# Kernel optimization log

Measured on AMD Instinct MI355X. Metric: run time of the kernel, lower is better.

The kernel has to match this reference:

```python
import jax, jax.numpy as jnp
import numpy as np

N_NODES = 20000
IN_C = 512
OUT_C = 128
HEADS = 4
N_EDGES = 320000
NEG_SLOPE = 0.2


def setup_inputs() -> dict:
    key = jax.random.key(0)
    ks = jax.random.split(key, 10)
    x = jax.random.normal(ks[0], (N_NODES, IN_C), dtype=jnp.float32)
    edge_index = jax.random.randint(ks[1], (2, N_EDGES), 0, N_NODES, dtype=jnp.int64)
    s = 0.05
    return {
        "x": x,
        "edge_index": edge_index,
        "W1": jax.random.normal(ks[2], (IN_C, HEADS * OUT_C), dtype=jnp.float32) * s,
        "a_src1": jax.random.normal(ks[3], (HEADS, OUT_C), dtype=jnp.float32) * s,
        "a_dst1": jax.random.normal(ks[4], (HEADS, OUT_C), dtype=jnp.float32) * s,
        "b1": jnp.zeros((HEADS * OUT_C,), dtype=jnp.float32),
        "W2": jax.random.normal(ks[5], (HEADS * OUT_C, 1 * OUT_C), dtype=jnp.float32) * s,
        "a_src2": jax.random.normal(ks[6], (1, OUT_C), dtype=jnp.float32) * s,
        "a_dst2": jax.random.normal(ks[7], (1, OUT_C), dtype=jnp.float32) * s,
        "b2": jnp.zeros((OUT_C,), dtype=jnp.float32),
    }


def gat_conv(x, src, dst, W, a_src, a_dst, b, heads, out_c, concat):
    N = x.shape[0]
    h = (x @ W).reshape(N, heads, out_c)            # [N,H,C]
    al_src = jnp.sum(h * a_src, axis=-1)            # [N,H]
    al_dst = jnp.sum(h * a_dst, axis=-1)            # [N,H]
    e = jax.nn.leaky_relu(al_src[src] + al_dst[dst], NEG_SLOPE)  # [E,H]
    # segment softmax over edges grouped by destination node
    e_max = jax.ops.segment_max(e, dst, num_segments=N)         # [N,H]
    e = jnp.exp(e - e_max[dst])
    denom = jax.ops.segment_sum(e, dst, num_segments=N)         # [N,H]
    alpha = e / (denom[dst] + 1e-16)                             # [E,H]
    msg = h[src] * alpha[:, :, None]                             # [E,H,C]
    out = jax.ops.segment_sum(msg, dst, num_segments=N)          # [N,H,C]
    out = out.reshape(N, heads * out_c) if concat else jnp.mean(out, axis=1)
    return out + b


def reference(x, edge_index, W1, a_src1, a_dst1, b1, W2, a_src2, a_dst2, b2):
    N = x.shape[0]
    # PyG GATConv adds self-loops by default
    loops = jnp.arange(N, dtype=edge_index.dtype)
    src = jnp.concatenate([edge_index[0], loops])
    dst = jnp.concatenate([edge_index[1], loops])
    h = gat_conv(x, src, dst, W1, a_src1, a_dst1, b1, HEADS, OUT_C, concat=True)
    h = jax.nn.elu(h)
    return gat_conv(h, src, dst, W2, a_src2, a_dst2, b2, 1, OUT_C, concat=False)
```

## Files before the change

### kernel.cpp

```cpp
#include <hip/hip_runtime.h>
#include <hip/hip_bf16.h>

typedef __hip_bfloat16 bf16;
typedef __bf16 bf16x8 __attribute__((ext_vector_type(8)));
typedef float f32x4 __attribute__((ext_vector_type(4)));

#define NEG_SLOPE 0.2f
#define F32_THRESH 256


__device__ __forceinline__ bool is_f32(const int* fcnt) { return *fcnt > F32_THRESH; }

__device__ __forceinline__ float ld_f(const void* p, long long i, bool f32) {
    return f32 ? ((const float*)p)[i] : __bfloat162float(((const bf16*)p)[i]);
}

__device__ __forceinline__ float b2f(unsigned hs) {
    return __uint_as_float(hs << 16);
}

__device__ __forceinline__ unsigned pack_bf2(float a, float b) {
    union { bf16 h[2]; unsigned u; } p;
    p.h[0] = __float2bfloat16(a);
    p.h[1] = __float2bfloat16(b);
    return p.u;
}

__device__ __forceinline__ void load_lds16(const void* g, void* l) {
    __builtin_amdgcn_global_load_lds(
        (const __attribute__((address_space(1))) void*)g,
        (__attribute__((address_space(3))) void*)l, 16, 0, 0);
}

template <int CPL> struct FV;
template <> struct FV<8> {
    uint4 v;
    __device__ __forceinline__ void load(const bf16* p) { v = *(const uint4*)p; }
    __device__ __forceinline__ void fma(float* acc, float w) const {
        unsigned uu[4] = {v.x, v.y, v.z, v.w};
#pragma unroll
        for (int q = 0; q < 4; q++) {
            acc[2 * q] += w * b2f(uu[q] & 0xFFFFu);
            acc[2 * q + 1] += w * b2f(uu[q] >> 16);
        }
    }
};
template <> struct FV<2> {
    unsigned v;
    __device__ __forceinline__ void load(const bf16* p) { v = *(const unsigned*)p; }
    __device__ __forceinline__ void fma(float* acc, float w) const {
        acc[0] += w * b2f(v & 0xFFFFu);
        acc[1] += w * b2f(v >> 16);
    }
};


__global__ void k_probe(const unsigned* xw, long long nw, const int* idx, int n_half,
                        int* cnt, int* iflag) {
    long long t = blockIdx.x * (long long)blockDim.x + threadIdx.x;
    long long stride = (long long)gridDim.x * blockDim.x;
    int c = 0;
    for (long long i = t; i < nw; i += stride)
        if ((xw[i] & 0x7F80u) == 0x7F80u) c++;
    if (c) atomicAdd(cnt, c);
    int any = 0;
    for (long long i = t; i < n_half; i += stride)
        if (idx[2 * i + 1] != 0) any = 1;
    if (any) atomicOr(iflag, 1);
}


__device__ __forceinline__ int edge_val(const void* idx, long long i, int is64) {
    return is64 ? (int)((const long long*)idx)[i] : ((const int*)idx)[i];
}

__global__ void k_count(const void* idx, const int* iflag, int E0, int N, int* deg) {
    int e = blockIdx.x * blockDim.x + threadIdx.x;
    if (e >= E0 + N) return;
    int is64 = (*iflag == 0);
    int d = (e < E0) ? edge_val(idx, (long long)E0 + e, is64) : (e - E0);
    if ((unsigned)d >= (unsigned)N) d = 0;
    atomicAdd(&deg[d], 1);
}

__global__ __launch_bounds__(1024) void k_scan(const int* deg, int* rowptr, int N) {
    __shared__ int part[1024];
    int t = threadIdx.x;
    int chunk = (N + 1023) / 1024;
    int s = t * chunk, e = min(N, s + chunk);
    int sum = 0;
    for (int i = s; i < e; i++) sum += deg[i];
    part[t] = sum;
    __syncthreads();
    for (int off = 1; off < 1024; off <<= 1) {
        int v = (t >= off) ? part[t - off] : 0;
        __syncthreads();
        part[t] += v;
        __syncthreads();
    }
    int run = (t == 0) ? 0 : part[t - 1];
    for (int i = s; i < e; i++) { rowptr[i] = run; run += deg[i]; }
    if (t == 1023) rowptr[N] = part[1023];
}

__global__ void k_scatter(const void* idx, const int* iflag, int E0, int N,
                          const int* rowptr, int* cursor, int* csr_src) {
    int e = blockIdx.x * blockDim.x + threadIdx.x;
    if (e >= E0 + N) return;
    int is64 = (*iflag == 0);
    int s, d;
    if (e < E0) {
        s = edge_val(idx, e, is64);
        d = edge_val(idx, (long long)E0 + e, is64);
    } else {
        s = d = e - E0;
    }
    if ((unsigned)s >= (unsigned)N) s = 0;
    if ((unsigned)d >= (unsigned)N) d = 0;
    int pos = rowptr[d] + atomicAdd(&cursor[d], 1);
    if ((unsigned)pos < (unsigned)(E0 + N)) csr_src[pos] = s;
}


__global__ void k_prep(const void* x, const int* fcnt, bf16* xb, bf16* xtail,
                       const void* W1, bf16* W1t, const void* W2, bf16* W2t,
                       bf16* hpad, int hpad_elems, int N, int K, int C1, int C2,
                       int R0, long long n_valid, long long n_total) {
    const int b = blockIdx.x;
    const int tid = threadIdx.x;
    const bool f32 = is_f32(fcnt);
    if (b < 512) {
        if (!f32) return;
        long long n8 = n_total / 8;
        for (long long i = (long long)b * 256 + tid; i < n8; i += 512LL * 256) {
            long long base = i * 8;
            uint4 out;
            if (base + 8 <= n_valid) {
                const float4* s4 = (const float4*)x;
                float4 x0 = s4[i * 2], x1 = s4[i * 2 + 1];
                out.x = pack_bf2(x0.x, x0.y);
                out.y = pack_bf2(x0.z, x0.w);
                out.z = pack_bf2(x1.x, x1.y);
                out.w = pack_bf2(x1.z, x1.w);
            } else {
                bf16 tmp[8];
#pragma unroll
                for (int j = 0; j < 8; j++) {
                    long long k = base + j;
                    tmp[j] = (k < n_valid) ? __float2bfloat16(ld_f(x, k, true))
                                           : __float2bfloat16(0.f);
                }
                out = *(uint4*)tmp;
            }
            ((uint4*)xb)[i] = out;
        }
    } else if (b < 528) {
        int total = 128 * K;
        for (int i = (b - 512) * 256 + tid; i < total; i += 16 * 256) {
            int r = i / K;
            long long src = (long long)(R0 + r) * K + (i - r * K);
            xtail[i] = (R0 + r < N) ? __float2bfloat16(ld_f(x, src, f32))
                                    : __float2bfloat16(0.f);
        }
    } else if (b < 656) {
        int total = K * C1;
        for (int i = (b - 528) * 256 + tid; i < total; i += 128 * 256) {
            int k = i / C1, n = i - k * C1;
            W1t[(size_t)n * K + k] = __float2bfloat16(ld_f(W1, i, f32));
        }
    } else if (b < 688) {
        int total = C1 * C2;
        for (int i = (b - 656) * 256 + tid; i < total; i += 32 * 256) {
            int k = i / C2, n = i - k * C2;
            W2t[(size_t)n * C1 + k] = __float2bfloat16(ld_f(W2, i, f32));
        }
    } else {
        for (int i = (b - 688) * 256 + tid; i < hpad_elems; i += 16 * 256)
            hpad[i] = __float2bfloat16(0.f);
    }
}


template <int BN, bool SEL, int H>
__global__ __launch_bounds__(256) void k_gemm(const void* Araw, const bf16* Aconv,
                                              const bf16* Atail, const int* fcnt,
                                              const bf16* __restrict__ Bt,
                                              bf16* __restrict__ C,
                                              const void* a_s, const void* a_d,
                                              float* __restrict__ als,
                                              float* __restrict__ ald,
                                              int M, int Nn, int K, int nfull) {
    constexpr int BM = 128, BK = 32;
    constexpr int NT = BN / 32;
    const int m0 = blockIdx.x * BM;
    const int n0 = blockIdx.y * BN;
    __shared__ __bf16 As[BM][BK];
    __shared__ __bf16 Bs[BN][BK];
    const int tid = threadIdx.x;
    const int wave = tid >> 6;
    const int lane = tid & 63;
    const int wm = (wave & 1) * 64;
    const int wn = (wave >> 1) * (NT * 16);
    const int lm = lane & 15;
    const int quad = lane >> 4;
    const int srow = tid >> 2;
    const int scol = (tid & 3) * 8;

    f32x4 acc[4][NT];
#pragma unroll
    for (int mt = 0; mt < 4; mt++)
#pragma unroll
        for (int nt = 0; nt < NT; nt++) acc[mt][nt] = (f32x4){0.f, 0.f, 0.f, 0.f};

    const bf16* Abase;
    int arow0;
    if (SEL) {
        const bf16* Asel = is_f32(fcnt) ? Aconv : (const bf16*)Araw;
        if ((int)blockIdx.x < nfull) { Abase = Asel; arow0 = m0; }
        else { Abase = Atail; arow0 = 0; }
    } else {
        Abase = (const bf16*)Araw;
        arow0 = m0;
    }

    const char* Ab = (const char*)(Abase + (size_t)(arow0 + srow) * K + scol);
    const char* Bb = (const char*)(Bt + (size_t)(n0 + srow) * K + scol);
    char* ldsA = (char*)&As[0][0] + wave * 1024;
    char* ldsB = (char*)&Bs[0][0] + wave * 1024;
    const size_t rstep = (size_t)64 * K * 2;

    for (int k0 = 0; k0 < K; k0 += BK) {
        __syncthreads();
        const size_t kb = (size_t)k0 * 2;
        load_lds16(Ab + kb, ldsA);
        load_lds16(Ab + kb + rstep, ldsA + 4096);
        load_lds16(Bb + kb, ldsB);
        if (BN == 128) load_lds16(Bb + kb + rstep, ldsB + 4096);
        __syncthreads();
        bf16x8 af[4], bfv[NT];
#pragma unroll
        for (int mt = 0; mt < 4; mt++)
            af[mt] = *(const bf16x8*)&As[wm + mt * 16 + lm][quad * 8];
#pragma unroll
        for (int nt = 0; nt < NT; nt++)
            bfv[nt] = *(const bf16x8*)&Bs[wn + nt * 16 + lm][quad * 8];
#pragma unroll
        for (int mt = 0; mt < 4; mt++)
#pragma unroll
            for (int nt = 0; nt < NT; nt++)
                acc[mt][nt] = __builtin_amdgcn_mfma_f32_16x16x32_bf16(
                    af[mt], bfv[nt], acc[mt][nt], 0, 0, 0);
    }

#pragma unroll
    for (int mt = 0; mt < 4; mt++) {
        int rb = m0 + wm + mt * 16 + quad * 4;
#pragma unroll
        for (int nt = 0; nt < NT; nt++) {
            int col = n0 + wn + nt * 16 + lm;
#pragma unroll
            for (int r = 0; r < 4; r++) {
                int row = rb + r;
                if (row < M) C[(size_t)row * Nn + col] = __float2bfloat16(acc[mt][nt][r]);
            }
        }
    }

    const bool f32 = is_f32(fcnt);
    float sa_[NT], sd_[NT];
#pragma unroll
    for (int nt = 0; nt < NT; nt++) {
        int col = n0 + wn + nt * 16 + lm;
        sa_[nt] = ld_f(a_s, col, f32);
        sd_[nt] = ld_f(a_d, col, f32);
    }
    const int head = (H == 4) ? (n0 >> 7) : 0;
#pragma unroll
    for (int mt = 0; mt < 4; mt++) {
#pragma unroll
        for (int r = 0; r < 4; r++) {
            float ps_ = 0.f, pd_ = 0.f;
#pragma unroll
            for (int nt = 0; nt < NT; nt++) {
                float v = acc[mt][nt][r];
                ps_ += v * sa_[nt];
                pd_ += v * sd_[nt];
            }
#pragma unroll
            for (int off = 1; off < 16; off <<= 1) {
                ps_ += __shfl_xor(ps_, off, 64);
                pd_ += __shfl_xor(pd_, off, 64);
            }
            int row = m0 + wm + mt * 16 + quad * 4 + r;
            if (lm == 0 && row < M) {
                atomicAdd(&als[(size_t)row * H + head], ps_);
                atomicAdd(&ald[(size_t)row * H + head], pd_);
            }
        }
    }
}


template <int C, int H, bool ELU, bool DYN_OUT>
__global__ __launch_bounds__(256) void k_agg(
    const bf16* __restrict__ feat, const float* __restrict__ als,
    const float* __restrict__ ald, const int* __restrict__ rowptr,
    const int* __restrict__ csr_src, const void* bias, const int* fcnt,
    void* outp, int N, int E) {
    constexpr int CPL = C / 64;
    constexpr int Ch = C / H;
    constexpr int WST = (H == 4) ? 5 : 1;
    const int n = blockIdx.x;
    const int tid = threadIdx.x;
    const int wave = tid >> 6;
    const int lane = tid & 63;
    const int c0 = lane * CPL;
    const int head = c0 / Ch;

    __shared__ float red[4][C];
    __shared__ float s_w[64 * WST];
    __shared__ int s_src[64];
    __shared__ float ps[4][H];

    int start = rowptr[n];
    if (start < 0) start = 0;
    int end = rowptr[n + 1];
    if (end > E) end = E;
    int deg = end - start;
    if (deg < 0) deg = 0;

    float acc[CPL] = {};
    float psum = 0.f;

    for (int base = 0; base < deg; base += 64) {
        int cnt = min(64, deg - base);
        __syncthreads();
        if (H == 4) {
            int e_ = tid & 63, h_ = tid >> 6;
            if (e_ < cnt) {
                int s = csr_src[start + base + e_];
                if ((unsigned)s >= (unsigned)N) s = 0;
                if (h_ == 0) s_src[e_] = s;
                float l = als[(size_t)s * 4 + h_] + ald[(size_t)n * 4 + h_];
                l = l > 0.f ? l : NEG_SLOPE * l;
                s_w[e_ * 5 + h_] = __expf(fminf(l, 60.f));
            }
        } else {
            if (tid < cnt) {
                int s = csr_src[start + base + tid];
                if ((unsigned)s >= (unsigned)N) s = 0;
                s_src[tid] = s;
                float l = als[s] + ald[n];
                l = l > 0.f ? l : NEG_SLOPE * l;
                s_w[tid] = __expf(fminf(l, 60.f));
            }
        }
        __syncthreads();
#pragma unroll 4
        for (int e = wave; e < cnt; e += 4) {
            int s = s_src[e];
            float wl = (H == 4) ? s_w[e * 5 + head] : s_w[e];
            psum += wl;
            FV<CPL> f;
            f.load(feat + (size_t)s * C + c0);
            f.fma(acc, wl);
        }
    }

#pragma unroll
    for (int j = 0; j < CPL; j++) red[wave][c0 + j] = acc[j];
    if ((lane & 15) == 0) ps[wave][head] = psum;
    __syncthreads();

    const bool f32 = is_f32(fcnt);
    for (int c = tid; c < C; c += 256) {
        int h = c / Ch;
        float sv = 0.f;
        float dn = 1e-16f;
#pragma unroll
        for (int w2 = 0; w2 < 4; w2++) {
            sv += red[w2][c];
            dn += ps[w2][h];
        }
        float v = sv / dn + ld_f(bias, c, f32);
        if (ELU) v = v > 0.f ? v : expf(v) - 1.f;
        size_t oi = (size_t)n * C + c;
        if (DYN_OUT && f32) ((float*)outp)[oi] = v;
        else ((bf16*)outp)[oi] = __float2bfloat16(v);
    }
}


extern "C" void kernel_launch(void* const* d_in, const int* in_sizes, int n_in,
                              void* d_out, int out_size, void* d_ws, size_t ws_size,
                              hipStream_t stream) {
    const int N = in_sizes[0] / 512;
    const int K = 512;
    const int C1 = 512;
    const int C2 = 128;
    const int H1 = 4;
    const int E0 = in_sizes[1] / 2;
    const int E = E0 + N;
    const int Mpad = (N + 127) / 128 * 128;
    const int nfull = N / 128;

    const void* x_raw = d_in[0];
    const void* eidx = d_in[1];
    const void* W1 = d_in[2];
    const void* as1 = d_in[3];
    const void* ad1 = d_in[4];
    const void* b1 = d_in[5];
    const void* W2 = d_in[6];
    const void* as2 = d_in[7];
    const void* ad2 = d_in[8];
    const void* b2 = d_in[9];

    char* ws = (char*)d_ws;
    size_t off = 0;
    auto take = [&](size_t bytes) {
        size_t r = off;
        off += (bytes + 255) & ~(size_t)255;
        return r;
    };
    bf16* xb     = (bf16*)(ws + take((size_t)Mpad * K * 2));
    bf16* xtail  = (bf16*)(ws + take((size_t)128 * K * 2));
    bf16* h1     = (bf16*)(ws + take((size_t)N * C1 * 2));
    bf16* hagg   = (bf16*)(ws + take((size_t)Mpad * C1 * 2));
    bf16* W1t    = (bf16*)(ws + take((size_t)K * C1 * 2));
    bf16* W2t    = (bf16*)(ws + take((size_t)C1 * C2 * 2));
    int* rowptr  = (int*)(ws + take((size_t)(N + 1) * 4));
    int* csr_src = (int*)(ws + take((size_t)E * 4));
    int* zbase   = (int*)(ws + take((size_t)(12 * N + 2) * 4));
    int* deg     = zbase;
    int* cursor  = zbase + N;
    float* al1s  = (float*)(zbase + 2 * N);
    float* al1d  = al1s + 4 * N;
    float* al2s  = al1d + 4 * N;
    float* al2d  = al2s + N;
    int* iflag   = zbase + 12 * N;
    int* fcnt    = zbase + 12 * N + 1;
    bf16* h2     = xb;
    if (off > ws_size) return;

    hipMemsetAsync(zbase, 0, (size_t)(12 * N + 2) * 4, stream);

    long long nw = (long long)in_sizes[0] / 2;
    if (nw > (1 << 20)) nw = 1 << 20;
    int nh = E0 > (1 << 16) ? (1 << 16) : E0;
    k_probe<<<256, 256, 0, stream>>>((const unsigned*)x_raw, nw, (const int*)eidx, nh,
                                     fcnt, iflag);

    k_count<<<(E + 255) / 256, 256, 0, stream>>>(eidx, iflag, E0, N, deg);
    k_scan<<<1, 1024, 0, stream>>>(deg, rowptr, N);
    k_scatter<<<(E + 255) / 256, 256, 0, stream>>>(eidx, iflag, E0, N, rowptr, cursor,
                                                   csr_src);

    k_prep<<<704, 256, 0, stream>>>(x_raw, fcnt, xb, xtail, W1, W1t, W2, W2t,
                                    hagg + (size_t)N * C1, (Mpad - N) * C1,
                                    N, K, C1, C2, nfull * 128,
                                    (long long)N * K, (long long)Mpad * K);

    dim3 g1(Mpad / 128, C1 / 128);
    k_gemm<128, true, 4><<<g1, 256, 0, stream>>>(x_raw, xb, xtail, fcnt, W1t, h1,
                                                 as1, ad1, al1s, al1d, N, C1, K, nfull);
    k_agg<512, 4, true, false><<<N, 256, 0, stream>>>(
        h1, al1s, al1d, rowptr, csr_src, b1, fcnt, hagg, N, E);

    dim3 g2(Mpad / 128, C2 / 64);
    k_gemm<64, false, 1><<<g2, 256, 0, stream>>>(hagg, nullptr, nullptr, fcnt, W2t, h2,
                                                 as2, ad2, al2s, al2d, N, C2, C1, 0);
    k_agg<128, 1, false, true><<<N, 256, 0, stream>>>(
        h2, al2s, al2d, rowptr, csr_src, b2, fcnt, d_out, N, E);
}
```

Before: 327.0 us.

## Fuse whole GAT pipeline into one cooperative persistent kernel with grid syncs

Replaces the sequence of separate launches (memset, probe, count, scan, scatter, prep, two GEMMs, two aggregations) with a single cooperative kernel that runs each phase in turn, separated by grid-wide barriers. The scan becomes a distributed block-sum plus single-block prefix. The goal is to remove per-launch overhead and inter-kernel gaps. The trade-off is that occupancy is capped by the shared-memory and register footprint of the largest phase, the grid is limited to resident blocks, and every phase waits on a full grid barrier, with the old multi-kernel path kept as a fallback.

```diff
diff --git a/kernel.cpp b/kernel.cpp
--- a/kernel.cpp
+++ b/kernel.cpp
@@ -1,5 +1,8 @@
 #include <hip/hip_runtime.h>
 #include <hip/hip_bf16.h>
+#include <hip/hip_cooperative_groups.h>
+
+namespace cg = cooperative_groups;
 
 typedef __hip_bfloat16 bf16;
 typedef __bf16 bf16x8 __attribute__((ext_vector_type(8)));
@@ -53,6 +56,415 @@
         acc[1] += w * b2f(v >> 16);
     }
 };
+
+__device__ __forceinline__ int edge_val(const void* idx, long long i, int is64) {
+    return is64 ? (int)((const long long*)idx)[i] : ((const int*)idx)[i];
+}
+
+
+template <int BN, bool SEL, int H>
+__device__ void dev_gemm(char* smem, int bx, int by,
+                         const void* Araw, const bf16* Aconv, const bf16* Atail,
+                         const int* fcnt, const bf16* __restrict__ Bt,
+                         bf16* __restrict__ C, const void* a_s, const void* a_d,
+                         float* __restrict__ als, float* __restrict__ ald,
+                         int M, int Nn, int K, int nfull) {
+    constexpr int BM = 128, BK = 32;
+    constexpr int NT = BN / 32;
+    const int m0 = bx * BM;
+    const int n0 = by * BN;
+    __bf16* As = (__bf16*)smem;
+    __bf16* Bs = (__bf16*)(smem + 8192);
+    const int tid = threadIdx.x;
+    const int wave = tid >> 6;
+    const int lane = tid & 63;
+    const int wm = (wave & 1) * 64;
+    const int wn = (wave >> 1) * (NT * 16);
+    const int lm = lane & 15;
+    const int quad = lane >> 4;
+    const int srow = tid >> 2;
+    const int scol = (tid & 3) * 8;
+
+    f32x4 acc[4][NT];
+#pragma unroll
+    for (int mt = 0; mt < 4; mt++)
+#pragma unroll
+        for (int nt = 0; nt < NT; nt++) acc[mt][nt] = (f32x4){0.f, 0.f, 0.f, 0.f};
+
+    const bf16* Abase;
+    int arow0;
+    if (SEL) {
+        const bf16* Asel = is_f32(fcnt) ? Aconv : (const bf16*)Araw;
+        if (bx < nfull) { Abase = Asel; arow0 = m0; }
+        else { Abase = Atail; arow0 = 0; }
+    } else {
+        Abase = (const bf16*)Araw;
+        arow0 = m0;
+    }
+
+    const char* Ab = (const char*)(Abase + (size_t)(arow0 + srow) * K + scol);
+    const char* Bb = (const char*)(Bt + (size_t)(n0 + srow) * K + scol);
+    char* ldsA = (char*)As + wave * 1024;
+    char* ldsB = (char*)Bs + wave * 1024;
+    const size_t rstep = (size_t)64 * K * 2;
+
+    for (int k0 = 0; k0 < K; k0 += BK) {
+        __syncthreads();
+        const size_t kb = (size_t)k0 * 2;
+        load_lds16(Ab + kb, ldsA);
+        load_lds16(Ab + kb + rstep, ldsA + 4096);
+        load_lds16(Bb + kb, ldsB);
+        if (BN == 128) load_lds16(Bb + kb + rstep, ldsB + 4096);
+        __syncthreads();
+        bf16x8 af[4], bfv[NT];
+#pragma unroll
+        for (int mt = 0; mt < 4; mt++)
+            af[mt] = *(const bf16x8*)(As + (wm + mt * 16 + lm) * 32 + quad * 8);
+#pragma unroll
+        for (int nt = 0; nt < NT; nt++)
+            bfv[nt] = *(const bf16x8*)(Bs + (wn + nt * 16 + lm) * 32 + quad * 8);
+#pragma unroll
+        for (int mt = 0; mt < 4; mt++)
+#pragma unroll
+            for (int nt = 0; nt < NT; nt++)
+                acc[mt][nt] = __builtin_amdgcn_mfma_f32_16x16x32_bf16(
+                    af[mt], bfv[nt], acc[mt][nt], 0, 0, 0);
+    }
+
+#pragma unroll
+    for (int mt = 0; mt < 4; mt++) {
+        int rb = m0 + wm + mt * 16 + quad * 4;
+#pragma unroll
+        for (int nt = 0; nt < NT; nt++) {
+            int col = n0 + wn + nt * 16 + lm;
+#pragma unroll
+            for (int r = 0; r < 4; r++) {
+                int row = rb + r;
+                if (row < M) C[(size_t)row * Nn + col] = __float2bfloat16(acc[mt][nt][r]);
+            }
+        }
+    }
+
+    const bool f32 = is_f32(fcnt);
+    float sa_[NT], sd_[NT];
+#pragma unroll
+    for (int nt = 0; nt < NT; nt++) {
+        int col = n0 + wn + nt * 16 + lm;
+        sa_[nt] = ld_f(a_s, col, f32);
+        sd_[nt] = ld_f(a_d, col, f32);
+    }
+    const int head = (H == 4) ? (n0 >> 7) : 0;
+#pragma unroll
+    for (int mt = 0; mt < 4; mt++) {
+#pragma unroll
+        for (int r = 0; r < 4; r++) {
+            float ps_ = 0.f, pd_ = 0.f;
+#pragma unroll
+            for (int nt = 0; nt < NT; nt++) {
+                float v = acc[mt][nt][r];
+                ps_ += v * sa_[nt];
+                pd_ += v * sd_[nt];
+            }
+#pragma unroll
+            for (int off = 1; off < 16; off <<= 1) {
+                ps_ += __shfl_xor(ps_, off, 64);
+                pd_ += __shfl_xor(pd_, off, 64);
+            }
+            int row = m0 + wm + mt * 16 + quad * 4 + r;
+            if (lm == 0 && row < M) {
+                atomicAdd(&als[(size_t)row * H + head], ps_);
+                atomicAdd(&ald[(size_t)row * H + head], pd_);
+            }
+        }
+    }
+}
+
+template <int C, int H, bool ELU, bool DYN_OUT>
+__device__ void dev_agg(char* smem, int n, const bf16* __restrict__ feat,
+                        const float* __restrict__ als, const float* __restrict__ ald,
+                        const int* __restrict__ rowptr, const int* __restrict__ csr_src,
+                        const void* bias, const int* fcnt, void* outp, int N, int E) {
+    constexpr int CPL = C / 64;
+    constexpr int Ch = C / H;
+    constexpr int WST = (H == 4) ? 5 : 1;
+    float* red = (float*)smem;
+    float* s_w = red + 4 * C;
+    int* s_src = (int*)(s_w + 64 * WST);
+    float* ps = (float*)(s_src + 64);
+    const int tid = threadIdx.x;
+    const int wave = tid >> 6;
+    const int lane = tid & 63;
+    const int c0 = lane * CPL;
+    const int head = c0 / Ch;
+
+    int start = rowptr[n];
+    if (start < 0) start = 0;
+    int end = rowptr[n + 1];
+    if (end > E) end = E;
+    int deg = end - start;
+    if (deg < 0) deg = 0;
+
+    float acc[CPL] = {};
+    float psum = 0.f;
+
+    for (int base = 0; base < deg; base += 64) {
+        int cnt = min(64, deg - base);
+        __syncthreads();
+        if (H == 4) {
+            int e_ = tid & 63, h_ = tid >> 6;
+            if (e_ < cnt) {
+                int s = csr_src[start + base + e_];
+                if ((unsigned)s >= (unsigned)N) s = 0;
+                if (h_ == 0) s_src[e_] = s;
+                float l = als[(size_t)s * 4 + h_] + ald[(size_t)n * 4 + h_];
+                l = l > 0.f ? l : NEG_SLOPE * l;
+                s_w[e_ * 5 + h_] = __expf(fminf(l, 60.f));
+            }
+        } else {
+            if (tid < cnt) {
+                int s = csr_src[start + base + tid];
+                if ((unsigned)s >= (unsigned)N) s = 0;
+                s_src[tid] = s;
+                float l = als[s] + ald[n];
+                l = l > 0.f ? l : NEG_SLOPE * l;
+                s_w[tid] = __expf(fminf(l, 60.f));
+            }
+        }
+        __syncthreads();
+#pragma unroll 4
+        for (int e = wave; e < cnt; e += 4) {
+            int s = s_src[e];
+            float wl = (H == 4) ? s_w[e * 5 + head] : s_w[e];
+            psum += wl;
+            FV<CPL> f;
+            f.load(feat + (size_t)s * C + c0);
+            f.fma(acc, wl);
+        }
+    }
+
+    __syncthreads();
+#pragma unroll
+    for (int j = 0; j < CPL; j++) red[wave * C + c0 + j] = acc[j];
+    if ((lane & 15) == 0) ps[wave * H + head] = psum;
+    __syncthreads();
+
+    const bool f32 = is_f32(fcnt);
+    for (int c = tid; c < C; c += 256) {
+        int h = c / Ch;
+        float sv = 0.f;
+        float dn = 1e-16f;
+#pragma unroll
+        for (int w2 = 0; w2 < 4; w2++) {
+            sv += red[w2 * C + c];
+            dn += ps[w2 * H + h];
+        }
+        float v = sv / dn + ld_f(bias, c, f32);
+        if (ELU) v = v > 0.f ? v : expf(v) - 1.f;
+        size_t oi = (size_t)n * C + c;
+        if (DYN_OUT && f32) ((float*)outp)[oi] = v;
+        else ((bf16*)outp)[oi] = __float2bfloat16(v);
+    }
+}
+
+
+struct MegaArgs {
+    const void* x_raw; const void* eidx;
+    const void* W1; const void* as1; const void* ad1; const void* b1;
+    const void* W2; const void* as2; const void* ad2; const void* b2;
+    bf16* xb; bf16* xtail; bf16* h1; bf16* hagg; bf16* W1t; bf16* W2t;
+    int* rowptr; int* csr_src; int* zbase; int* bsum;
+    void* out;
+    int N, K, C1, C2, E0, E, Mpad, nfull;
+    long long nw_cap; int nh_cap;
+};
+
+__global__ __launch_bounds__(256) void k_mega(MegaArgs a) {
+    cg::grid_group grid = cg::this_grid();
+    __shared__ __align__(16) char smem[16640];
+
+    const int blk = blockIdx.x;
+    const int tid = threadIdx.x;
+    const int G = gridDim.x;
+    const long long gt = (long long)blk * 256 + tid;
+    const long long GT = (long long)G * 256;
+
+    const int N = a.N, K = a.K, C1 = a.C1, C2 = a.C2;
+    const int E0 = a.E0, E = a.E, Mpad = a.Mpad, nfull = a.nfull;
+    int* deg = a.zbase;
+    int* cursor = a.zbase + N;
+    float* al1s = (float*)(a.zbase + 2 * N);
+    float* al1d = al1s + 4 * N;
+    float* al2s = al1d + 4 * N;
+    float* al2d = al2s + N;
+    int* iflag = a.zbase + 12 * N;
+    int* fcnt = a.zbase + 12 * N + 1;
+    bf16* h2 = a.xb;
+
+    {
+        long long zn = 12LL * N + 2;
+        for (long long i = gt; i < zn; i += GT) a.zbase[i] = 0;
+        unsigned* hp = (unsigned*)(a.hagg + (size_t)N * C1);
+        long long pw = (long long)(Mpad - N) * C1 / 2;
+        for (long long i = gt; i < pw; i += GT) hp[i] = 0;
+    }
+    grid.sync();
+
+    {
+        const unsigned* xw = (const unsigned*)a.x_raw;
+        int c = 0;
+        for (long long i = gt; i < a.nw_cap; i += GT)
+            if ((xw[i] & 0x7F80u) == 0x7F80u) c++;
+        if (c) atomicAdd(fcnt, c);
+        const int* idx = (const int*)a.eidx;
+        int any = 0;
+        for (long long i = gt; i < a.nh_cap; i += GT)
+            if (idx[2 * i + 1] != 0) any = 1;
+        if (any) atomicOr(iflag, 1);
+    }
+    grid.sync();
+
+    {
+        const int is64 = (*iflag == 0);
+        const bool f32 = is_f32(fcnt);
+        for (long long e = gt; e < E; e += GT) {
+            int d = (e < E0) ? edge_val(a.eidx, (long long)E0 + e, is64) : (int)(e - E0);
+            if ((unsigned)d >= (unsigned)N) d = 0;
+            atomicAdd(&deg[d], 1);
+        }
+        for (long long i = gt; i < (long long)K * C1; i += GT) {
+            int k = (int)(i / C1), n = (int)(i - (long long)k * C1);
+            a.W1t[(size_t)n * K + k] = __float2bfloat16(ld_f(a.W1, i, f32));
+        }
+        for (long long i = gt; i < (long long)C1 * C2; i += GT) {
+            int k = (int)(i / C2), n = (int)(i - (long long)k * C2);
+            a.W2t[(size_t)n * C1 + k] = __float2bfloat16(ld_f(a.W2, i, f32));
+        }
+        if (f32) {
+            long long n8 = (long long)Mpad * K / 8;
+            long long nv = (long long)N * K;
+            for (long long i = gt; i < n8; i += GT) {
+                long long base = i * 8;
+                uint4 out;
+                if (base + 8 <= nv) {
+                    const float4* s4 = (const float4*)a.x_raw;
+                    float4 x0 = s4[i * 2], x1 = s4[i * 2 + 1];
+                    out.x = pack_bf2(x0.x, x0.y);
+                    out.y = pack_bf2(x0.z, x0.w);
+                    out.z = pack_bf2(x1.x, x1.y);
+                    out.w = pack_bf2(x1.z, x1.w);
+                } else {
+                    bf16 tmp[8];
+#pragma unroll
+                    for (int j = 0; j < 8; j++) {
+                        long long kk = base + j;
+                        tmp[j] = (kk < nv) ? __float2bfloat16(ld_f(a.x_raw, kk, true))
+                                           : __float2bfloat16(0.f);
+                    }
+                    out = *(uint4*)tmp;
+                }
+                ((uint4*)a.xb)[i] = out;
+            }
+        }
+        int R0 = nfull * 128;
+        for (long long i = gt; i < (long long)128 * K; i += GT) {
+            int r = (int)(i / K);
+            long long src = (long long)(R0 + r) * K + (i - (long long)r * K);
+            a.xtail[i] = (R0 + r < N) ? __float2bfloat16(ld_f(a.x_raw, src, f32))
+                                      : __float2bfloat16(0.f);
+        }
+    }
+    grid.sync();
+
+    const int CH = (N + G - 1) / G;
+    const int cb = blk * CH;
+    const int ce = min(N, cb + CH);
+    {
+        int* ss = (int*)smem;
+        int local = 0;
+        for (int i = cb + tid; i < ce; i += 256) local += deg[i];
+        ss[tid] = local;
+        __syncthreads();
+        for (int s = 128; s > 0; s >>= 1) {
+            if (tid < s) ss[tid] += ss[tid + s];
+            __syncthreads();
+        }
+        if (tid == 0) a.bsum[blk] = ss[0];
+    }
+    grid.sync();
+
+    if (blk == 0) {
+        int* ss = (int*)smem;
+        int per = (G + 255) / 256;
+        int b0 = tid * per, b1 = min(G, b0 + per);
+        int s = 0;
+        for (int i = b0; i < b1; i++) s += a.bsum[i];
+        ss[tid] = s;
+        __syncthreads();
+        for (int off = 1; off < 256; off <<= 1) {
+            int x = (tid >= off) ? ss[tid - off] : 0;
+            __syncthreads();
+            ss[tid] += x;
+            __syncthreads();
+        }
+        int run = ss[tid] - s;
+        for (int i = b0; i < b1; i++) {
+            int v = a.bsum[i];
+            a.bsum[i] = run;
+            run += v;
+        }
+        if (tid == 255) a.rowptr[N] = ss[255];
+    }
+    grid.sync();
+
+    if (tid == 0) {
+        int run = a.bsum[blk];
+        for (int i = cb; i < ce; i++) { a.rowptr[i] = run; run += deg[i]; }
+    }
+    grid.sync();
+
+    {
+        const int is64 = (*iflag == 0);
+        for (long long e = gt; e < E; e += GT) {
+            int s, d;
+            if (e < E0) {
+                s = edge_val(a.eidx, e, is64);
+                d = edge_val(a.eidx, (long long)E0 + e, is64);
+            } else {
+                s = d = (int)(e - E0);
+            }
+            if ((unsigned)s >= (unsigned)N) s = 0;
+            if ((unsigned)d >= (unsigned)N) d = 0;
+            int pos = a.rowptr[d] + atomicAdd(&cursor[d], 1);
+            if ((unsigned)pos < (unsigned)E) a.csr_src[pos] = s;
+        }
+        const int mt1 = Mpad / 128;
+        const int nb1 = mt1 * (C1 / 128);
+        for (int t = blk; t < nb1; t += G)
+            dev_gemm<128, true, 4>(smem, t % mt1, t / mt1, a.x_raw, a.xb, a.xtail,
+                                   fcnt, a.W1t, a.h1, a.as1, a.ad1, al1s, al1d,
+                                   N, C1, K, nfull);
+    }
+    grid.sync();
+
+    for (int n = blk; n < N; n += G)
+        dev_agg<512, 4, true, false>(smem, n, a.h1, al1s, al1d, a.rowptr,
+                                     a.csr_src, a.b1, fcnt, a.hagg, N, E);
+    grid.sync();
+
+    {
+        const int mt1 = Mpad / 128;
+        const int nb2 = mt1 * (C2 / 64);
+        for (int t = blk; t < nb2; t += G)
+            dev_gemm<64, false, 1>(smem, t % mt1, t / mt1, a.hagg, nullptr, nullptr,
+                                   fcnt, a.W2t, h2, a.as2, a.ad2, al2s, al2d,
+                                   N, C2, C1, 0);
+    }
+    grid.sync();
+
+    for (int n = blk; n < N; n += G)
+        dev_agg<128, 1, false, true>(smem, n, h2, al2s, al2d, a.rowptr,
+                                     a.csr_src, a.b2, fcnt, a.out, N, E);
+}
 
 
 __global__ void k_probe(const unsigned* xw, long long nw, const int* idx, int n_half,
@@ -67,11 +479,6 @@
     for (long long i = t; i < n_half; i += stride)
         if (idx[2 * i + 1] != 0) any = 1;
     if (any) atomicOr(iflag, 1);
-}
-
-
-__device__ __forceinline__ int edge_val(const void* idx, long long i, int is64) {
-    return is64 ? (int)((const long long*)idx)[i] : ((const int*)idx)[i];
 }
 
 __global__ void k_count(const void* idx, const int* iflag, int E0, int N, int* deg) {
@@ -120,7 +527,6 @@
     int pos = rowptr[d] + atomicAdd(&cursor[d], 1);
     if ((unsigned)pos < (unsigned)(E0 + N)) csr_src[pos] = s;
 }
-
 
 __global__ void k_prep(const void* x, const int* fcnt, bf16* xb, bf16* xtail,
                        const void* W1, bf16* W1t, const void* W2, bf16* W2t,
@@ -180,214 +586,28 @@
     }
 }
 
-
 template <int BN, bool SEL, int H>
-__global__ __launch_bounds__(256) void k_gemm(const void* Araw, const bf16* Aconv,
-                                              const bf16* Atail, const int* fcnt,
-                                              const bf16* __restrict__ Bt,
-                                              bf16* __restrict__ C,
-                                              const void* a_s, const void* a_d,
-                                              float* __restrict__ als,
-                                              float* __restrict__ ald,
-                                              int M, int Nn, int K, int nfull) {
-    constexpr int BM = 128, BK = 32;
-    constexpr int NT = BN / 32;
-    const int m0 = blockIdx.x * BM;
-    const int n0 = blockIdx.y * BN;
-    __shared__ __bf16 As[BM][BK];
-    __shared__ __bf16 Bs[BN][BK];
-    const int tid = threadIdx.x;
-    const int wave = tid >> 6;
-    const int lane = tid & 63;
-    const int wm = (wave & 1) * 64;
-    const int wn = (wave >> 1) * (NT * 16);
-    const int lm = lane & 15;
-    const int quad = lane >> 4;
-    const int srow = tid >> 2;
-    const int scol = (tid & 3) * 8;
-
-    f32x4 acc[4][NT];
-#pragma unroll
-    for (int mt = 0; mt < 4; mt++)
-#pragma unroll
-        for (int nt = 0; nt < NT; nt++) acc[mt][nt] = (f32x4){0.f, 0.f, 0.f, 0.f};
-
-    const bf16* Abase;
-    int arow0;
-    if (SEL) {
-        const bf16* Asel = is_f32(fcnt) ? Aconv : (const bf16*)Araw;
-        if ((int)blockIdx.x < nfull) { Abase = Asel; arow0 = m0; }
-        else { Abase = Atail; arow0 = 0; }
-    } else {
-        Abase = (const bf16*)Araw;
-        arow0 = m0;
-    }
-
-    const char* Ab = (const char*)(Abase + (size_t)(arow0 + srow) * K + scol);
-    const char* Bb = (const char*)(Bt + (size_t)(n0 + srow) * K + scol);
-    char* ldsA = (char*)&As[0][0] + wave * 1024;
-    char* ldsB = (char*)&Bs[0][0] + wave * 1024;
-    const size_t rstep = (size_t)64 * K * 2;
-
-    for (int k0 = 0; k0 < K; k0 += BK) {
-        __syncthreads();
-        const size_t kb = (size_t)k0 * 2;
-        load_lds16(Ab + kb, ldsA);
-        load_lds16(Ab + kb + rstep, ldsA + 4096);
-        load_lds16(Bb + kb, ldsB);
-        if (BN == 128) load_lds16(Bb + kb + rstep, ldsB + 4096);
-        __syncthreads();
-        bf16x8 af[4], bfv[NT];
-#pragma unroll
-        for (int mt = 0; mt < 4; mt++)
-            af[mt] = *(const bf16x8*)&As[wm + mt * 16 + lm][quad * 8];
-#pragma unroll
-        for (int nt = 0; nt < NT; nt++)
-            bfv[nt] = *(const bf16x8*)&Bs[wn + nt * 16 + lm][quad * 8];
-#pragma unroll
-        for (int mt = 0; mt < 4; mt++)
-#pragma unroll
-            for (int nt = 0; nt < NT; nt++)
-                acc[mt][nt] = __builtin_amdgcn_mfma_f32_16x16x32_bf16(
-                    af[mt], bfv[nt], acc[mt][nt], 0, 0, 0);
-    }
-
-#pragma unroll
-    for (int mt = 0; mt < 4; mt++) {
-        int rb = m0 + wm + mt * 16 + quad * 4;
-#pragma unroll
-        for (int nt = 0; nt < NT; nt++) {
-            int col = n0 + wn + nt * 16 + lm;
-#pragma unroll
-            for (int r = 0; r < 4; r++) {
-                int row = rb + r;
-                if (row < M) C[(size_t)row * Nn + col] = __float2bfloat16(acc[mt][nt][r]);
-            }
-        }
-    }
-
-    const bool f32 = is_f32(fcnt);
-    float sa_[NT], sd_[NT];
-#pragma unroll
-    for (int nt = 0; nt < NT; nt++) {
-        int col = n0 + wn + nt * 16 + lm;
-        sa_[nt] = ld_f(a_s, col, f32);
-        sd_[nt] = ld_f(a_d, col, f32);
-    }
-    const int head = (H == 4) ? (n0 >> 7) : 0;
-#pragma unroll
-    for (int mt = 0; mt < 4; mt++) {
-#pragma unroll
-        for (int r = 0; r < 4; r++) {
-            float ps_ = 0.f, pd_ = 0.f;
-#pragma unroll
-            for (int nt = 0; nt < NT; nt++) {
-                float v = acc[mt][nt][r];
-                ps_ += v * sa_[nt];
-                pd_ += v * sd_[nt];
-            }
-#pragma unroll
-            for (int off = 1; off < 16; off <<= 1) {
-                ps_ += __shfl_xor(ps_, off, 64);
-                pd_ += __shfl_xor(pd_, off, 64);
-            }
-            int row = m0 + wm + mt * 16 + quad * 4 + r;
-            if (lm == 0 && row < M) {
-                atomicAdd(&als[(size_t)row * H + head], ps_);
-                atomicAdd(&ald[(size_t)row * H + head], pd_);
-            }
-        }
-    }
-}
-
+__global__ __launch_bounds__(256) void k_gemm_w(const void* Araw, const bf16* Aconv,
+                                                const bf16* Atail, const int* fcnt,
+                                                const bf16* Bt, bf16* C,
+                                                const void* a_s, const void* a_d,
+                                                float* als, float* ald,
+                                                int M, int Nn, int K, int nfull) {
+    __shared__ __align__(16) char smem[128 * 32 * 2 + BN * 32 * 2];
+    dev_gemm<BN, SEL, H>(smem, blockIdx.x, blockIdx.y, Araw, Aconv, Atail, fcnt,
+                         Bt, C, a_s, a_d, als, ald, M, Nn, K, nfull);
+}
 
 template <int C, int H, bool ELU, bool DYN_OUT>
-__global__ __launch_bounds__(256) void k_agg(
-    const bf16* __restrict__ feat, const float* __restrict__ als,
-    const float* __restrict__ ald, const int* __restrict__ rowptr,
-    const int* __restrict__ csr_src, const void* bias, const int* fcnt,
-    void* outp, int N, int E) {
-    constexpr int CPL = C / 64;
-    constexpr int Ch = C / H;
-    constexpr int WST = (H == 4) ? 5 : 1;
-    const int n = blockIdx.x;
-    const int tid = threadIdx.x;
-    const int wave = tid >> 6;
-    const int lane = tid & 63;
-    const int c0 = lane * CPL;
-    const int head = c0 / Ch;
-
-    __shared__ float red[4][C];
-    __shared__ float s_w[64 * WST];
-    __shared__ int s_src[64];
-    __shared__ float ps[4][H];
-
-    int start = rowptr[n];
-    if (start < 0) start = 0;
-    int end = rowptr[n + 1];
-    if (end > E) end = E;
-    int deg = end - start;
-    if (deg < 0) deg = 0;
-
-    float acc[CPL] = {};
-    float psum = 0.f;
-
-    for (int base = 0; base < deg; base += 64) {
-        int cnt = min(64, deg - base);
-        __syncthreads();
-        if (H == 4) {
-            int e_ = tid & 63, h_ = tid >> 6;
-            if (e_ < cnt) {
-                int s = csr_src[start + base + e_];
-                if ((unsigned)s >= (unsigned)N) s = 0;
-                if (h_ == 0) s_src[e_] = s;
-                float l = als[(size_t)s * 4 + h_] + ald[(size_t)n * 4 + h_];
-                l = l > 0.f ? l : NEG_SLOPE * l;
-                s_w[e_ * 5 + h_] = __expf(fminf(l, 60.f));
-            }
-        } else {
-            if (tid < cnt) {
-                int s = csr_src[start + base + tid];
-                if ((unsigned)s >= (unsigned)N) s = 0;
-                s_src[tid] = s;
-                float l = als[s] + ald[n];
-                l = l > 0.f ? l : NEG_SLOPE * l;
-                s_w[tid] = __expf(fminf(l, 60.f));
-            }
-        }
-        __syncthreads();
-#pragma unroll 4
-        for (int e = wave; e < cnt; e += 4) {
-            int s = s_src[e];
-            float wl = (H == 4) ? s_w[e * 5 + head] : s_w[e];
-            psum += wl;
-            FV<CPL> f;
-            f.load(feat + (size_t)s * C + c0);
-            f.fma(acc, wl);
-        }
-    }
-
-#pragma unroll
-    for (int j = 0; j < CPL; j++) red[wave][c0 + j] = acc[j];
-    if ((lane & 15) == 0) ps[wave][head] = psum;
-    __syncthreads();
-
-    const bool f32 = is_f32(fcnt);
-    for (int c = tid; c < C; c += 256) {
-        int h = c / Ch;
-        float sv = 0.f;
-        float dn = 1e-16f;
-#pragma unroll
-        for (int w2 = 0; w2 < 4; w2++) {
-            sv += red[w2][c];
-            dn += ps[w2][h];
-        }
-        float v = sv / dn + ld_f(bias, c, f32);
-        if (ELU) v = v > 0.f ? v : expf(v) - 1.f;
-        size_t oi = (size_t)n * C + c;
-        if (DYN_OUT && f32) ((float*)outp)[oi] = v;
-        else ((bf16*)outp)[oi] = __float2bfloat16(v);
-    }
+__global__ __launch_bounds__(256) void k_agg_w(const bf16* feat, const float* als,
+                                               const float* ald, const int* rowptr,
+                                               const int* csr_src, const void* bias,
+                                               const int* fcnt, void* outp,
+                                               int N, int E) {
+    __shared__ __align__(16) char
+        smem[4 * C * 4 + 64 * ((H == 4) ? 5 : 1) * 4 + 64 * 4 + 4 * H * 4];
+    dev_agg<C, H, ELU, DYN_OUT>(smem, blockIdx.x, feat, als, ald, rowptr, csr_src,
+                                bias, fcnt, outp, N, E);
 }
 
 
@@ -398,22 +618,10 @@
     const int K = 512;
     const int C1 = 512;
     const int C2 = 128;
-    const int H1 = 4;
     const int E0 = in_sizes[1] / 2;
     const int E = E0 + N;
     const int Mpad = (N + 127) / 128 * 128;
     const int nfull = N / 128;
-
-    const void* x_raw = d_in[0];
-    const void* eidx = d_in[1];
-    const void* W1 = d_in[2];
-    const void* as1 = d_in[3];
-    const void* ad1 = d_in[4];
-    const void* b1 = d_in[5];
-    const void* W2 = d_in[6];
-    const void* as2 = d_in[7];
-    const void* ad2 = d_in[8];
-    const void* b2 = d_in[9];
 
     char* ws = (char*)d_ws;
     size_t off = 0;
@@ -431,44 +639,74 @@
     int* rowptr  = (int*)(ws + take((size_t)(N + 1) * 4));
     int* csr_src = (int*)(ws + take((size_t)E * 4));
     int* zbase   = (int*)(ws + take((size_t)(12 * N + 2) * 4));
-    int* deg     = zbase;
-    int* cursor  = zbase + N;
-    float* al1s  = (float*)(zbase + 2 * N);
-    float* al1d  = al1s + 4 * N;
-    float* al2s  = al1d + 4 * N;
-    float* al2d  = al2s + N;
-    int* iflag   = zbase + 12 * N;
-    int* fcnt    = zbase + 12 * N + 1;
-    bf16* h2     = xb;
+    int* bsum    = (int*)(ws + take((size_t)4096 * 4));
     if (off > ws_size) return;
 
+    MegaArgs a;
+    a.x_raw = d_in[0]; a.eidx = d_in[1];
+    a.W1 = d_in[2]; a.as1 = d_in[3]; a.ad1 = d_in[4]; a.b1 = d_in[5];
+    a.W2 = d_in[6]; a.as2 = d_in[7]; a.ad2 = d_in[8]; a.b2 = d_in[9];
+    a.xb = xb; a.xtail = xtail; a.h1 = h1; a.hagg = hagg;
+    a.W1t = W1t; a.W2t = W2t;
+    a.rowptr = rowptr; a.csr_src = csr_src; a.zbase = zbase; a.bsum = bsum;
+    a.out = d_out;
+    a.N = N; a.K = K; a.C1 = C1; a.C2 = C2;
+    a.E0 = E0; a.E = E; a.Mpad = Mpad; a.nfull = nfull;
+    long long nw = (long long)in_sizes[0] / 2;
+    a.nw_cap = nw > (1 << 20) ? (1 << 20) : nw;
+    a.nh_cap = E0 > (1 << 16) ? (1 << 16) : E0;
+
+    int dev = 0;
+    hipGetDevice(&dev);
+    int coop = 0, numCU = 0, nbPerCU = 0;
+    hipDeviceGetAttribute(&coop, hipDeviceAttributeCooperativeLaunch, dev);
+    hipDeviceGetAttribute(&numCU, hipDeviceAttributeMultiprocessorCount, dev);
+    hipError_t oe = hipOccupancyMaxActiveBlocksPerMultiprocessor(
+        &nbPerCU, reinterpret_cast<const void*>(&k_mega), 256, 0);
+
+    if (coop && oe == hipSuccess && nbPerCU >= 1 && numCU >= 1) {
+        int G = nbPerCU * numCU;
+        if (G > 4096) G = 4096;
+        void* params[] = {&a};
+        hipError_t e = hipLaunchCooperativeKernel(
+            reinterpret_cast<const void*>(&k_mega), dim3(G), dim3(256),
+            params, 0, stream);
+        if (e == hipSuccess) return;
+    }
+
+    float* al1s = (float*)(zbase + 2 * N);
+    float* al1d = al1s + 4 * N;
+    float* al2s = al1d + 4 * N;
+    float* al2d = al2s + N;
+    int* deg = zbase;
+    int* cursor = zbase + N;
+    int* iflag = zbase + 12 * N;
+    int* fcnt = zbase + 12 * N + 1;
+    bf16* h2 = xb;
+
     hipMemsetAsync(zbase, 0, (size_t)(12 * N + 2) * 4, stream);
-
-    long long nw = (long long)in_sizes[0] / 2;
-    if (nw > (1 << 20)) nw = 1 << 20;
-    int nh = E0 > (1 << 16) ? (1 << 16) : E0;
-    k_probe<<<256, 256, 0, stream>>>((const unsigned*)x_raw, nw, (const int*)eidx, nh,
-                                     fcnt, iflag);
-
-    k_count<<<(E + 255) / 256, 256, 0, stream>>>(eidx, iflag, E0, N, deg);
+    k_probe<<<256, 256, 0, stream>>>((const unsigned*)a.x_raw, a.nw_cap,
+                                     (const int*)a.eidx, a.nh_cap, fcnt, iflag);
+    k_count<<<(E + 255) / 256, 256, 0, stream>>>(a.eidx, iflag, E0, N, deg);
     k_scan<<<1, 1024, 0, stream>>>(deg, rowptr, N);
-    k_scatter<<<(E + 255) / 256, 256, 0, stream>>>(eidx, iflag, E0, N, rowptr, cursor,
-                                                   csr_src);
-
-    k_prep<<<704, 256, 0, stream>>>(x_raw, fcnt, xb, xtail, W1, W1t, W2, W2t,
+    k_scatter<<<(E + 255) / 256, 256, 0, stream>>>(a.eidx, iflag, E0, N, rowptr,
+                                                   cursor, csr_src);
+    k_prep<<<704, 256, 0, stream>>>(a.x_raw, fcnt, xb, xtail, a.W1, W1t, a.W2, W2t,
                                     hagg + (size_t)N * C1, (Mpad - N) * C1,
                                     N, K, C1, C2, nfull * 128,
                                     (long long)N * K, (long long)Mpad * K);
-
     dim3 g1(Mpad / 128, C1 / 128);
-    k_gemm<128, true, 4><<<g1, 256, 0, stream>>>(x_raw, xb, xtail, fcnt, W1t, h1,
-                                                 as1, ad1, al1s, al1d, N, C1, K, nfull);
-    k_agg<512, 4, true, false><<<N, 256, 0, stream>>>(
-        h1, al1s, al1d, rowptr, csr_src, b1, fcnt, hagg, N, E);
-
+    k_gemm_w<128, true, 4><<<g1, 256, 0, stream>>>(a.x_raw, xb, xtail, fcnt, W1t, h1,
+                                                   a.as1, a.ad1, al1s, al1d,
+                                                   N, C1, K, nfull);
+    k_agg_w<512, 4, true, false><<<N, 256, 0, stream>>>(h1, al1s, al1d, rowptr,
+                                                        csr_src, a.b1, fcnt, hagg,
+                                                        N, E);
     dim3 g2(Mpad / 128, C2 / 64);
-    k_gemm<64, false, 1><<<g2, 256, 0, stream>>>(hagg, nullptr, nullptr, fcnt, W2t, h2,
-                                                 as2, ad2, al2s, al2d, N, C2, C1, 0);
-    k_agg<128, 1, false, true><<<N, 256, 0, stream>>>(
-        h2, al2s, al2d, rowptr, csr_src, b2, fcnt, d_out, N, E);
-}
+    k_gemm_w<64, false, 1><<<g2, 256, 0, stream>>>(hagg, nullptr, nullptr, fcnt, W2t,
+                                                   h2, a.as2, a.ad2, al2s, al2d,
+                                                   N, C2, C1, 0);
+    k_agg_w<128, 1, false, true><<<N, 256, 0, stream>>>(h2, al2s, al2d, rowptr,
+                                                        csr_src, a.b2, fcnt, d_out,
+                                                        N, E);
+}
```

New measurement: 349.1 us. 6.8% more time.
